# Kernel tuning notes

Hardware: AMD Instinct MI355X
Metric: run time of the kernel (lower is better)

The kernel has to match this reference:

```python
import jax, jax.numpy as jnp
import numpy as np

N = 80000    # total nodes
E = 640000   # total edges
B = 800      # graphs in batch
NPG = 100    # nodes per graph
HID = 128
NC = 10
IND = 20     # one-hot degree feature size (torch.eye(20))
EPS = 1e-5


def _gconv(x, src, dst, inv_out, inv_in, W, b):
    # DGL GraphConv, norm='both': D_out^{-1/2} scaling at src, sum-aggregate, D_in^{-1/2} at dst
    m = (x * inv_out[:, None])[src]                      # [E, F]
    agg = jax.ops.segment_sum(m, dst, num_segments=x.shape[0])
    return (agg * inv_in[:, None]) @ W + b


def _bn(x, gamma, beta):
    # BatchNorm1d, training-mode (batch statistics, biased variance)
    mu = x.mean(0)
    var = x.var(0)
    return (x - mu) / jnp.sqrt(var + EPS) * gamma + beta


def setup_inputs():
    key = jax.random.key(0)
    ks = jax.random.split(key, 10)
    # edges constrained within each graph (batched disjoint graphs, as in dgl.batch)
    eg = jax.random.randint(ks[0], (E,), 0, B)
    src = (eg * NPG + jax.random.randint(ks[1], (E,), 0, NPG)).astype(jnp.int32)
    dst = (eg * NPG + jax.random.randint(ks[2], (E,), 0, NPG)).astype(jnp.int32)
    graph_id = (jnp.arange(N) // NPG).astype(jnp.int32)

    def p(k, shape, fan):
        return (jax.random.normal(k, shape, jnp.float32) / np.sqrt(fan)).astype(jnp.float32)

    z = lambda s: jnp.zeros(s, jnp.float32)
    o = lambda s: jnp.ones(s, jnp.float32)
    return dict(
        src=src, dst=dst, graph_id=graph_id,
        W1=p(ks[3], (IND, HID), IND), b1=z((HID,)), g1=o((HID,)), be1=z((HID,)),
        W2=p(ks[4], (HID, HID), HID), b2=z((HID,)), g2=o((HID,)), be2=z((HID,)),
        Wv=p(ks[5], (HID, 1), HID), bv=z((1,)),
        Wd=p(ks[6], (1, HID), 1), bd=z((HID,)),
        Wg=p(ks[7], (HID, HID), HID), bg=z((HID,)), g3=o((HID,)), be3=z((HID,)),
        Wc=p(ks[8], (HID, NC), HID), bc=z((NC,)),
    )


def reference(src, dst, graph_id, W1, b1, g1, be1, W2, b2, g2, be2,
              Wv, bv, Wd, bd, Wg, bg, g3, be3, Wc, bc):
    n = graph_id.shape[0]
    ones_e = jnp.ones(src.shape[0], jnp.float32)
    in_deg = jax.ops.segment_sum(ones_e, dst, num_segments=n)
    out_deg = jax.ops.segment_sum(ones_e, src, num_segments=n)
    inv_in = jax.lax.rsqrt(jnp.maximum(in_deg, 1.0))   # DGL clamps deg min 1
    inv_out = jax.lax.rsqrt(jnp.maximum(out_deg, 1.0))

    # node features: one-hot of in-degree (eye(20)[in_degrees]); clip to valid range
    h = jax.nn.one_hot(jnp.clip(in_deg.astype(jnp.int32), 0, IND - 1), IND, dtype=jnp.float32)
    h = jax.nn.elu(_bn(_gconv(h, src, dst, inv_out, inv_in, W1, b1), g1, be1))  # [N,HID]
    h = jax.nn.elu(_bn(_gconv(h, src, dst, inv_out, inv_in, W2, b2), g2, be2))  # [N,HID]

    v = _gconv(h, src, dst, inv_out, inv_in, Wv, bv)   # [N,1], node weights d
    d = v[:, 0]

    # per-graph ragged matmul: vec_i = d_i^T @ h_i, done as one segment-sum
    vec = jax.ops.segment_sum(d[:, None] * h, graph_id, num_segments=B).reshape(-1)  # [B*HID]
    mean = vec.mean()
    vec = jax.nn.relu(vec - mean) - jax.nn.relu(-vec - mean)   # soft shrink by global mean

    hg = jnp.tanh(vec.reshape(B, HID))
    hg = jnp.tanh(_bn(hg @ Wg + bg, g3, be3))
    return jnp.tanh(hg @ Wc + bc)   # [B, NC] (eval-mode output)
```

## Files before the change

### kernel.cpp

```cpp
#include <hip/hip_runtime.h>
#include <hip/hip_bf16.h>
#include <math.h>

#define N_NODES 80000
#define N_EDGES 640000
#define B_GR 800
#define NPG 100
#define HID 128
#define NC 10
#define IND 20
#define BN_EPS 1e-5f

__global__ void k_A(const int* __restrict__ src, const int* __restrict__ dst,
                    unsigned int* A) {
    int e = blockIdx.x * blockDim.x + threadIdx.x;
    if (e < N_EDGES) {
        int s = src[e], d = dst[e];
        int g = d / NPG;
        int bidx = g * (NPG * NPG) + (d - g * NPG) * NPG + (s - g * NPG);
        atomicAdd(&A[bidx >> 2], 1u << ((bidx & 3) * 8));
    }
}

__global__ __launch_bounds__(128) void k_prep(const unsigned int* __restrict__ A,
                                              float* __restrict__ inv_in,
                                              float* __restrict__ inv_out,
                                              float* __restrict__ agg20) {
    __shared__ unsigned int s_A[NPG * 25];
    __shared__ float s_io[NPG];
    __shared__ int   s_ix[NPG];
    __shared__ float s_agg[NPG][IND + 1];
    int g = blockIdx.x, gbase = g * NPG, t = threadIdx.x;
    const unsigned int* Ag = A + g * 2500;
    for (int i = t; i < NPG * 25; i += 128) s_A[i] = Ag[i];
    __syncthreads();

    if (t < NPG) {
        int rsum = 0;
        const unsigned int* row = &s_A[t * 25];
#pragma unroll
        for (int q = 0; q < 25; ++q) {
            unsigned int c4 = row[q];
            rsum += (int)((c4 & 255u) + ((c4 >> 8) & 255u) + ((c4 >> 16) & 255u) + (c4 >> 24));
        }
        int csum = 0;
        int wq = t >> 2, sh = (t & 3) * 8;
#pragma unroll 4
        for (int r = 0; r < NPG; ++r)
            csum += (int)((s_A[r * 25 + wq] >> sh) & 255u);

        float io = rsqrtf(fmaxf((float)csum, 1.f));
        inv_in[gbase + t]  = rsqrtf(fmaxf((float)rsum, 1.f));
        inv_out[gbase + t] = io;
        s_io[t] = io;
        s_ix[t] = rsum > IND - 1 ? IND - 1 : rsum;
    }
    __syncthreads();

    if (t < NPG) {
#pragma unroll
        for (int k = 0; k < IND; ++k) s_agg[t][k] = 0.f;
        const unsigned int* row = &s_A[t * 25];
#pragma unroll
        for (int q = 0; q < 25; ++q) {
            unsigned int c4 = row[q];
            if (c4 == 0) continue;
#pragma unroll
            for (int b = 0; b < 4; ++b) {
                unsigned int cnt = (c4 >> (8 * b)) & 255u;
                if (cnt) {
                    int s = q * 4 + b;
                    s_agg[t][s_ix[s]] += (float)cnt * s_io[s];
                }
            }
        }
        float* outp = agg20 + (size_t)(gbase + t) * IND;
#pragma unroll
        for (int k = 0; k < IND; ++k) outp[k] = s_agg[t][k];
    }
}

#define MOM_CHUNK 64
__global__ __launch_bounds__(256) void k_mom(const float* __restrict__ agg20,
                                             const float* __restrict__ inv_in,
                                             float* s20, float* Mbuf) {
    __shared__ float rows[MOM_CHUNK * IND];
    __shared__ float w1s[MOM_CHUNK], w2s[MOM_CHUNK];
    int t = threadIdx.x;
    int k = 0, l = 0;
    bool isM = (t < 210), isS = (t >= 210 && t < 230);
    if (isM) {
        int idx = t, kk = 0;
        while (idx >= IND - kk) { idx -= IND - kk; ++kk; }
        k = kk; l = kk + idx;
    } else if (isS) {
        k = t - 210;
    }
    float acc = 0.f;
    for (int c = blockIdx.x; c < N_NODES / MOM_CHUNK; c += gridDim.x) {
        __syncthreads();
        for (int i = t * 4; i < MOM_CHUNK * IND; i += 1024)
            *(float4*)&rows[i] = *(const float4*)&agg20[(size_t)c * MOM_CHUNK * IND + i];
        if (t < MOM_CHUNK) {
            float v = inv_in[c * MOM_CHUNK + t];
            w1s[t] = v; w2s[t] = v * v;
        }
        __syncthreads();
        if (isM) {
            for (int i = 0; i < MOM_CHUNK; ++i)
                acc += w2s[i] * rows[i * IND + k] * rows[i * IND + l];
        } else if (isS) {
            for (int i = 0; i < MOM_CHUNK; ++i)
                acc += w1s[i] * rows[i * IND + k];
        }
    }
    if (isM) atomicAdd(&Mbuf[t], acc);
    else if (isS) atomicAdd(&s20[t - 210], acc);
}

__global__ void k_bn1fin(const float* __restrict__ s20, const float* __restrict__ Mbuf,
                         const float* __restrict__ W1, const float* __restrict__ b1,
                         const float* __restrict__ g1, const float* __restrict__ be1,
                         float* a1, float* c1) {
    __shared__ float sM[210], ss[IND];
    int j = threadIdx.x;
    if (j < 210) sM[j] = Mbuf[j];
    if (j + 128 < 210) sM[j + 128] = Mbuf[j + 128];
    if (j < IND) ss[j] = s20[j];
    __syncthreads();
    float w[IND];
#pragma unroll
    for (int k = 0; k < IND; ++k) w[k] = W1[k * HID + j];
    float tj = 0.f;
#pragma unroll
    for (int k = 0; k < IND; ++k) tj += ss[k] * w[k];
    float q = 0.f;
    int idx = 0;
#pragma unroll
    for (int k = 0; k < IND; ++k) {
        q += sM[idx] * w[k] * w[k]; ++idx;
#pragma unroll
        for (int l = k + 1; l < IND; ++l) { q += 2.f * sM[idx] * w[k] * w[l]; ++idx; }
    }
    float bj = b1[j];
    const float Nf = (float)N_NODES;
    float mean = (tj + Nf * bj) / Nf;
    float ey2  = (q + 2.f * bj * tj + Nf * bj * bj) / Nf;
    float var  = ey2 - mean * mean;
    float aj = g1[j] / sqrtf(var + BN_EPS);
    a1[j] = aj;
    c1[j] = be1[j] - mean * aj;
}

__global__ __launch_bounds__(256) void k_l1f(const float* __restrict__ agg20,
                                             const float* __restrict__ inv_in,
                                             const float* __restrict__ inv_out,
                                             const float* __restrict__ W1,
                                             const float* __restrict__ b1,
                                             const float* __restrict__ a1,
                                             const float* __restrict__ c1,
                                             float* __restrict__ h1s) {
    __shared__ float ws[IND * HID];
    int t = threadIdx.x;
    for (int i = t * 4; i < IND * HID; i += 1024)
        *(float4*)&ws[i] = *(const float4*)&W1[i];
    __syncthreads();
    int tx = t & 15, ty = t >> 4;
    int c0 = tx * 8;
    float4 ba = *(const float4*)(b1 + c0);
    float4 bb = *(const float4*)(b1 + c0 + 4);
    float4 aa = *(const float4*)(a1 + c0);
    float4 ab = *(const float4*)(a1 + c0 + 4);
    float4 ca = *(const float4*)(c1 + c0);
    float4 cb = *(const float4*)(c1 + c0 + 4);

    int row0 = blockIdx.x * 64 + ty * 4;
    const float* xr0 = agg20 + (size_t)row0 * IND;
    const float* xr1 = xr0 + IND;
    const float* xr2 = xr1 + IND;
    const float* xr3 = xr2 + IND;
    float acc[4][8];
#pragma unroll
    for (int r = 0; r < 4; ++r)
#pragma unroll
        for (int c = 0; c < 8; ++c) acc[r][c] = 0.f;

#pragma unroll
    for (int k = 0; k < IND; k += 4) {
        float4 x0 = *(const float4*)(xr0 + k);
        float4 x1 = *(const float4*)(xr1 + k);
        float4 x2 = *(const float4*)(xr2 + k);
        float4 x3 = *(const float4*)(xr3 + k);
#pragma unroll
        for (int kk = 0; kk < 4; ++kk) {
            float4 wa = *(const float4*)&ws[(k + kk) * HID + c0];
            float4 wb = *(const float4*)&ws[(k + kk) * HID + c0 + 4];
            float xk0 = (kk == 0) ? x0.x : (kk == 1) ? x0.y : (kk == 2) ? x0.z : x0.w;
            float xk1 = (kk == 0) ? x1.x : (kk == 1) ? x1.y : (kk == 2) ? x1.z : x1.w;
            float xk2 = (kk == 0) ? x2.x : (kk == 1) ? x2.y : (kk == 2) ? x2.z : x2.w;
            float xk3 = (kk == 0) ? x3.x : (kk == 1) ? x3.y : (kk == 2) ? x3.z : x3.w;
            acc[0][0] += xk0 * wa.x; acc[0][1] += xk0 * wa.y;
            acc[0][2] += xk0 * wa.z; acc[0][3] += xk0 * wa.w;
            acc[0][4] += xk0 * wb.x; acc[0][5] += xk0 * wb.y;
            acc[0][6] += xk0 * wb.z; acc[0][7] += xk0 * wb.w;
            acc[1][0] += xk1 * wa.x; acc[1][1] += xk1 * wa.y;
            acc[1][2] += xk1 * wa.z; acc[1][3] += xk1 * wa.w;
            acc[1][4] += xk1 * wb.x; acc[1][5] += xk1 * wb.y;
            acc[1][6] += xk1 * wb.z; acc[1][7] += xk1 * wb.w;
            acc[2][0] += xk2 * wa.x; acc[2][1] += xk2 * wa.y;
            acc[2][2] += xk2 * wa.z; acc[2][3] += xk2 * wa.w;
            acc[2][4] += xk2 * wb.x; acc[2][5] += xk2 * wb.y;
            acc[2][6] += xk2 * wb.z; acc[2][7] += xk2 * wb.w;
            acc[3][0] += xk3 * wa.x; acc[3][1] += xk3 * wa.y;
            acc[3][2] += xk3 * wa.z; acc[3][3] += xk3 * wa.w;
            acc[3][4] += xk3 * wb.x; acc[3][5] += xk3 * wb.y;
            acc[3][6] += xk3 * wb.z; acc[3][7] += xk3 * wb.w;
        }
    }
    float4 iv = *(const float4*)(inv_in + row0);
    float4 ov = *(const float4*)(inv_out + row0);
#pragma unroll
    for (int r = 0; r < 4; ++r) {
        float ivr = (r == 0) ? iv.x : (r == 1) ? iv.y : (r == 2) ? iv.z : iv.w;
        float ovr = (r == 0) ? ov.x : (r == 1) ? ov.y : (r == 2) ? ov.z : ov.w;
        float y[8];
        y[0] = acc[r][0] * ivr + ba.x; y[1] = acc[r][1] * ivr + ba.y;
        y[2] = acc[r][2] * ivr + ba.z; y[3] = acc[r][3] * ivr + ba.w;
        y[4] = acc[r][4] * ivr + bb.x; y[5] = acc[r][5] * ivr + bb.y;
        y[6] = acc[r][6] * ivr + bb.z; y[7] = acc[r][7] * ivr + bb.w;
        float z[8];
        z[0] = y[0] * aa.x + ca.x; z[1] = y[1] * aa.y + ca.y;
        z[2] = y[2] * aa.z + ca.z; z[3] = y[3] * aa.w + ca.w;
        z[4] = y[4] * ab.x + cb.x; z[5] = y[5] * ab.y + cb.y;
        z[6] = y[6] * ab.z + cb.z; z[7] = y[7] * ab.w + cb.w;
#pragma unroll
        for (int c = 0; c < 8; ++c) {
            float h = z[c] > 0.f ? z[c] : expm1f(z[c]);
            z[c] = h * ovr;
        }
        float* yr = h1s + (size_t)(row0 + r) * HID + c0;
        *(float4*)yr = make_float4(z[0], z[1], z[2], z[3]);
        *(float4*)(yr + 4) = make_float4(z[4], z[5], z[6], z[7]);
    }
}

__global__ __launch_bounds__(512) void k_agg2v5(const unsigned int* __restrict__ A,
                                                const float* __restrict__ h1s,
                                                float* __restrict__ agg2) {
    __shared__ float sh[NPG * HID];
    int t = threadIdx.x;
    int g = blockIdx.x;
    int gbase = g * NPG;

    const float4* srcp = (const float4*)(h1s + (size_t)gbase * HID);
    float4* shp = (float4*)sh;
    for (int i = t; i < (NPG * HID) / 4; i += 512)
        shp[i] = srcp[i];
    __syncthreads();

    int wv = t >> 6, lane = t & 63;
    const unsigned int* Ag = A + g * 2500;
    for (int r = wv; r < NPG; r += 8) {
        const unsigned int* row = Ag + r * 25;
        unsigned int cq[25];
#pragma unroll
        for (int q = 0; q < 25; ++q) cq[q] = row[q];
        float ax = 0.f, ay = 0.f;
#pragma unroll
        for (int q = 0; q < 25; ++q) {
            unsigned int c4 = cq[q];
            if (c4 == 0) continue;
            int sbase = q * 4;
#pragma unroll
            for (int b = 0; b < 4; ++b) {
                unsigned int cnt = (c4 >> (8 * b)) & 255u;
                if (cnt) {
                    float f = (float)cnt;
                    float2 v = *(const float2*)&sh[(sbase + b) * HID + lane * 2];
                    ax += f * v.x; ay += f * v.y;
                }
            }
        }
        *(float2*)(agg2 + (size_t)(gbase + r) * HID + lane * 2) = make_float2(ax, ay);
    }
}

__global__ void k_bnfin(const float* sums, const float* sqs,
                        const float* gamma, const float* beta,
                        float cnt, float* a, float* c) {
    int j = threadIdx.x;
    float mu  = sums[j] / cnt;
    float var = sqs[j] / cnt - mu * mu;
    float aj  = gamma[j] / sqrtf(var + BN_EPS);
    a[j] = aj;
    c[j] = beta[j] - mu * aj;
}

__global__ __launch_bounds__(512) void k_l2v5(const float* __restrict__ xin,
                                              const float* __restrict__ inv_in,
                                              const float* __restrict__ W,
                                              const float* __restrict__ bvec,
                                              float* __restrict__ yout,
                                              float* sums, float* sqs) {
    __shared__ float ws[HID * 64];
    int t = threadIdx.x;
    int tile = blockIdx.x >> 1;
    int half = blockIdx.x & 1;
    int cbase = half * 64;
    for (int i = t; i < HID * 16; i += 512) {
        int k = i >> 4;
        int c4 = (i & 15) << 2;
        *(float4*)&ws[k * 64 + c4] = *(const float4*)&W[k * HID + cbase + c4];
    }
    __syncthreads();

    int tx = t & 15;
    int ty = t >> 4;
    int c0 = tx * 4;
    float4 ba = *(const float4*)(bvec + cbase + c0);
    float csum[4], csq[4];
#pragma unroll
    for (int c = 0; c < 4; ++c) { csum[c] = 0.f; csq[c] = 0.f; }

    int row0 = tile * 128 + ty * 4;
    const float* xr0 = xin + (size_t)row0 * HID;
    const float* xr1 = xr0 + HID;
    const float* xr2 = xr1 + HID;
    const float* xr3 = xr2 + HID;
    float acc[4][4];
#pragma unroll
    for (int r = 0; r < 4; ++r)
#pragma unroll
        for (int c = 0; c < 4; ++c) acc[r][c] = 0.f;

#pragma unroll 4
    for (int k = 0; k < HID; k += 4) {
        float4 x0 = *(const float4*)(xr0 + k);
        float4 x1 = *(const float4*)(xr1 + k);
        float4 x2 = *(const float4*)(xr2 + k);
        float4 x3 = *(const float4*)(xr3 + k);
#pragma unroll
        for (int kk = 0; kk < 4; ++kk) {
            float4 wa = *(const float4*)&ws[(k + kk) * 64 + c0];
            float xk0 = (kk == 0) ? x0.x : (kk == 1) ? x0.y : (kk == 2) ? x0.z : x0.w;
            float xk1 = (kk == 0) ? x1.x : (kk == 1) ? x1.y : (kk == 2) ? x1.z : x1.w;
            float xk2 = (kk == 0) ? x2.x : (kk == 1) ? x2.y : (kk == 2) ? x2.z : x2.w;
            float xk3 = (kk == 0) ? x3.x : (kk == 1) ? x3.y : (kk == 2) ? x3.z : x3.w;
            acc[0][0] += xk0 * wa.x; acc[0][1] += xk0 * wa.y;
            acc[0][2] += xk0 * wa.z; acc[0][3] += xk0 * wa.w;
            acc[1][0] += xk1 * wa.x; acc[1][1] += xk1 * wa.y;
            acc[1][2] += xk1 * wa.z; acc[1][3] += xk1 * wa.w;
            acc[2][0] += xk2 * wa.x; acc[2][1] += xk2 * wa.y;
            acc[2][2] += xk2 * wa.z; acc[2][3] += xk2 * wa.w;
            acc[3][0] += xk3 * wa.x; acc[3][1] += xk3 * wa.y;
            acc[3][2] += xk3 * wa.z; acc[3][3] += xk3 * wa.w;
        }
    }
    float4 iv = *(const float4*)(inv_in + row0);
#pragma unroll
    for (int r = 0; r < 4; ++r) {
        float ivr = (r == 0) ? iv.x : (r == 1) ? iv.y : (r == 2) ? iv.z : iv.w;
        float y0 = acc[r][0] * ivr + ba.x;
        float y1 = acc[r][1] * ivr + ba.y;
        float y2 = acc[r][2] * ivr + ba.z;
        float y3 = acc[r][3] * ivr + ba.w;
        csum[0] += y0; csq[0] += y0 * y0;
        csum[1] += y1; csq[1] += y1 * y1;
        csum[2] += y2; csq[2] += y2 * y2;
        csum[3] += y3; csq[3] += y3 * y3;
        *(float4*)(yout + (size_t)(row0 + r) * HID + cbase + c0) = make_float4(y0, y1, y2, y3);
    }

    __syncthreads();
#pragma unroll
    for (int c = 0; c < 4; ++c) {
        ws[ty * 64 + c0 + c] = csum[c];
        ws[2048 + ty * 64 + c0 + c] = csq[c];
    }
    __syncthreads();
    if (t < 64) {
        float s1 = 0.f, s2 = 0.f;
#pragma unroll
        for (int r = 0; r < 32; ++r) {
            s1 += ws[r * 64 + t];
            s2 += ws[2048 + r * 64 + t];
        }
        atomicAdd(&sums[cbase + t], s1);
        atomicAdd(&sqs[cbase + t], s2);
    }
}

__global__ __launch_bounds__(512) void k_post(const unsigned int* __restrict__ A,
                                              const float* __restrict__ y2,
                                              const float* __restrict__ a2,
                                              const float* __restrict__ c2,
                                              const float* __restrict__ inv_in,
                                              const float* __restrict__ inv_out,
                                              const float* __restrict__ Wv,
                                              const float* __restrict__ bv,
                                              float* __restrict__ vec,
                                              float* meansum) {
    __shared__ float sh[NPG * HID];
    __shared__ float s_p[NPG];
    __shared__ float s_d[NPG];
    __shared__ float s_red[512];
    int t = threadIdx.x;
    int g = blockIdx.x, gbase = g * NPG;

    const float4* srcp = (const float4*)(y2 + (size_t)gbase * HID);
    for (int i = t; i < (NPG * HID) / 4; i += 512) {
        int col = (i * 4) & (HID - 1);
        float4 v = srcp[i];
        float4 av = *(const float4*)(a2 + col);
        float4 cv = *(const float4*)(c2 + col);
        float z0 = v.x * av.x + cv.x; z0 = z0 > 0.f ? z0 : expm1f(z0);
        float z1 = v.y * av.y + cv.y; z1 = z1 > 0.f ? z1 : expm1f(z1);
        float z2 = v.z * av.z + cv.z; z2 = z2 > 0.f ? z2 : expm1f(z2);
        float z3 = v.w * av.w + cv.w; z3 = z3 > 0.f ? z3 : expm1f(z3);
        *(float4*)&sh[i * 4] = make_float4(z0, z1, z2, z3);
    }
    __syncthreads();

    int wv = t >> 6, lane = t & 63;
    float2 wvv = *(const float2*)(Wv + lane * 2);
    for (int r = wv; r < NPG; r += 8) {
        float2 h = *(const float2*)&sh[r * HID + lane * 2];
        float d = h.x * wvv.x + h.y * wvv.y;
        for (int off = 32; off; off >>= 1) d += __shfl_down(d, off);
        if (lane == 0) s_p[r] = d * inv_out[gbase + r];
    }
    __syncthreads();

    if (t < NPG) {
        const unsigned int* row = A + g * 2500 + t * 25;
        unsigned int cq[25];
#pragma unroll
        for (int q = 0; q < 25; ++q) cq[q] = row[q];
        float acc = 0.f;
#pragma unroll
        for (int q = 0; q < 25; ++q) {
            unsigned int c4 = cq[q];
            if (c4 == 0) continue;
#pragma unroll
            for (int b = 0; b < 4; ++b) {
                unsigned int cnt = (c4 >> (8 * b)) & 255u;
                if (cnt) acc += (float)cnt * s_p[q * 4 + b];
            }
        }
        s_d[t] = acc * inv_in[gbase + t] + bv[0];
    }
    __syncthreads();

    int col = t & (HID - 1);
    int qr = t >> 7;
    float part = 0.f;
    for (int r = qr * 25; r < qr * 25 + 25; ++r)
        part += s_d[r] * sh[r * HID + col];
    s_red[qr * HID + col] = part;
    __syncthreads();
    if (t < HID) {
        float v = s_red[t] + s_red[HID + t] + s_red[2 * HID + t] + s_red[3 * HID + t];
        vec[g * HID + t] = v;
        for (int off = 32; off; off >>= 1) v += __shfl_down(v, off);
        if ((t & 63) == 0) atomicAdd(meansum, v);
    }
}

__global__ __launch_bounds__(128) void k_g1(const float* __restrict__ vec,
                                            const float* __restrict__ meansum,
                                            const float* __restrict__ Wg,
                                            const float* __restrict__ bg,
                                            float* y3, float* sums, float* sqs) {
    __shared__ float ws[HID * HID];
    __shared__ float rows[HID];
    int g = blockIdx.x, j = threadIdx.x;
    for (int k = 0; k < HID; ++k) ws[k * HID + j] = Wg[k * HID + j];
    float mean = meansum[0] * (1.f / (B_GR * HID));
    float v = vec[g * HID + j];
    float sh = fmaxf(v - mean, 0.f) - fmaxf(-v - mean, 0.f);
    rows[j] = tanhf(sh);
    __syncthreads();
    float acc = 0.f;
#pragma unroll 8
    for (int k = 0; k < HID; ++k) acc += rows[k] * ws[k * HID + j];
    float y = acc + bg[j];
    y3[g * HID + j] = y;
    atomicAdd(&sums[j], y);
    atomicAdd(&sqs[j], y * y);
}

__global__ __launch_bounds__(128) void k_out(const float* __restrict__ y3,
                                             const float* __restrict__ a,
                                             const float* __restrict__ c,
                                             const float* __restrict__ Wc,
                                             const float* __restrict__ bc,
                                             float* out) {
    __shared__ float hg[HID];
    int g = blockIdx.x, j = threadIdx.x;
    hg[j] = tanhf(y3[g * HID + j] * a[j] + c[j]);
    __syncthreads();
    if (j < NC) {
        float acc = 0.f;
        for (int k = 0; k < HID; ++k) acc += hg[k] * Wc[k * NC + j];
        out[g * NC + j] = tanhf(acc + bc[j]);
    }
}

extern "C" void kernel_launch(void* const* d_in, const int* in_sizes, int n_in,
                              void* d_out, int out_size, void* d_ws, size_t ws_size,
                              hipStream_t stream) {
    const int*   src = (const int*)d_in[0];
    const int*   dst = (const int*)d_in[1];
    const float* W1  = (const float*)d_in[3];
    const float* b1  = (const float*)d_in[4];
    const float* g1  = (const float*)d_in[5];
    const float* be1 = (const float*)d_in[6];
    const float* W2  = (const float*)d_in[7];
    const float* b2  = (const float*)d_in[8];
    const float* g2  = (const float*)d_in[9];
    const float* be2 = (const float*)d_in[10];
    const float* Wv  = (const float*)d_in[11];
    const float* bv  = (const float*)d_in[12];
    const float* Wg  = (const float*)d_in[15];
    const float* bg  = (const float*)d_in[16];
    const float* g3  = (const float*)d_in[17];
    const float* be3 = (const float*)d_in[18];
    const float* Wc  = (const float*)d_in[19];
    const float* bc  = (const float*)d_in[20];
    float* out = (float*)d_out;

    char* ws = (char*)d_ws;
    size_t off = 0;
    auto carve = [&](size_t bytes) -> char* {
        char* pp = ws + off;
        off = (off + bytes + 255) & ~(size_t)255;
        return pp;
    };
    unsigned int* A = (unsigned int*)carve((size_t)B_GR * NPG * NPG);
    float* stats   = (float*)carve(2048 * 4);
    size_t zbytes = off;
    float* inv_in  = (float*)carve(N_NODES * 4);
    float* inv_out = (float*)carve(N_NODES * 4);
    float* vec     = (float*)carve((size_t)B_GR * HID * 4);
    float* y3      = (float*)carve((size_t)B_GR * HID * 4);
    float* agg20   = (float*)carve((size_t)N_NODES * IND * 4);
    float* bufA    = (float*)carve((size_t)N_NODES * HID * 4);
    float* bufB    = (float*)carve((size_t)N_NODES * HID * 4);

    float* sums2 = stats + 0;    float* sq2 = stats + 128;
    float* a2    = stats + 256;  float* c2  = stats + 384;
    float* sums3 = stats + 512;  float* sq3 = stats + 640;
    float* a3    = stats + 768;  float* c3  = stats + 896;
    float* meansum = stats + 1024;
    float* s20   = stats + 1056;
    float* Mbuf  = stats + 1088;
    float* a1    = stats + 1312;
    float* c1    = stats + 1440;

    hipMemsetAsync(d_ws, 0, zbytes, stream);

    k_A<<<(N_EDGES + 255) / 256, 256, 0, stream>>>(src, dst, A);
    k_prep<<<B_GR, 128, 0, stream>>>(A, inv_in, inv_out, agg20);
    k_mom<<<320, 256, 0, stream>>>(agg20, inv_in, s20, Mbuf);
    k_bn1fin<<<1, 128, 0, stream>>>(s20, Mbuf, W1, b1, g1, be1, a1, c1);
    k_l1f<<<N_NODES / 64, 256, 0, stream>>>(agg20, inv_in, inv_out, W1, b1, a1, c1, bufA);
    k_agg2v5<<<B_GR, 512, 0, stream>>>(A, bufA, bufB);
    k_l2v5<<<(N_NODES / 128) * 2, 512, 0, stream>>>(bufB, inv_in, W2, b2, bufA, sums2, sq2);
    k_bnfin<<<1, 128, 0, stream>>>(sums2, sq2, g2, be2, (float)N_NODES, a2, c2);
    k_post<<<B_GR, 512, 0, stream>>>(A, bufA, a2, c2, inv_in, inv_out, Wv, bv, vec, meansum);
    k_g1<<<B_GR, 128, 0, stream>>>(vec, meansum, Wg, bg, y3, sums3, sq3);
    k_bnfin<<<1, 128, 0, stream>>>(sums3, sq3, g3, be3, (float)B_GR, a3, c3);
    k_out<<<B_GR, 128, 0, stream>>>(y3, a3, c3, Wc, bc, out);
}
```

Before: 284.6 us.

## Run layer-2 GEMM on MFMA with split-bf16 (hi/lo) three-pass emulation

Replaces the FP32 SIMT 128x128 layer-2 matmul with an MFMA bf16 kernel. The aggregation kernel now writes its output as hi and lo bf16 halves, and W2 is pre-packed the same way into the MFMA operand layout. Three MFMAs (hi*hi, hi*lo, lo*hi) approximate FP32 accuracy. The aim is to cut the FP32 ALU cost of the GEMM while keeping memory traffic the same. The cost is an extra packing kernel, slightly lower precision, and per-element shared-memory atomics in the BN statistics reduction.

```diff
diff --git a/kernel.cpp b/kernel.cpp
--- a/kernel.cpp
+++ b/kernel.cpp
@@ -10,6 +10,18 @@
 #define NC 10
 #define IND 20
 #define BN_EPS 1e-5f
+
+typedef __attribute__((ext_vector_type(8))) short bf16x8;
+typedef __attribute__((ext_vector_type(4))) float f32x4;
+
+__device__ __forceinline__ unsigned short f2bf(float f) {
+    unsigned int u = __float_as_uint(f);
+    u = (u + 0x7fffu + ((u >> 16) & 1u)) >> 16;
+    return (unsigned short)u;
+}
+__device__ __forceinline__ float bf2f(unsigned short h) {
+    return __uint_as_float((unsigned int)h << 16);
+}
 
 __global__ void k_A(const int* __restrict__ src, const int* __restrict__ dst,
                     unsigned int* A) {
@@ -246,7 +258,8 @@
 
 __global__ __launch_bounds__(512) void k_agg2v5(const unsigned int* __restrict__ A,
                                                 const float* __restrict__ h1s,
-                                                float* __restrict__ agg2) {
+                                                unsigned short* __restrict__ agg2hi,
+                                                unsigned short* __restrict__ agg2lo) {
     __shared__ float sh[NPG * HID];
     int t = threadIdx.x;
     int g = blockIdx.x;
@@ -281,7 +294,102 @@
                 }
             }
         }
-        *(float2*)(agg2 + (size_t)(gbase + r) * HID + lane * 2) = make_float2(ax, ay);
+        unsigned short hx = f2bf(ax), hy = f2bf(ay);
+        unsigned short lx = f2bf(ax - bf2f(hx)), ly = f2bf(ay - bf2f(hy));
+        size_t o = (size_t)(gbase + r) * HID + lane * 2;
+        *(unsigned int*)(agg2hi + o) = (unsigned int)hx | ((unsigned int)hy << 16);
+        *(unsigned int*)(agg2lo + o) = (unsigned int)lx | ((unsigned int)ly << 16);
+    }
+}
+
+__global__ void k_wpack(const float* __restrict__ W2, unsigned short* __restrict__ Wpack) {
+    int i = blockIdx.x * 256 + threadIdx.x;
+    if (i < 16384) {
+        int j = i & 7, l = (i >> 3) & 63, kc = (i >> 9) & 3, nc = i >> 11;
+        int k = kc * 32 + 8 * (l >> 4) + j;
+        int n = nc * 16 + (l & 15);
+        float w = W2[k * HID + n];
+        unsigned short h = f2bf(w);
+        Wpack[i] = h;
+        Wpack[16384 + i] = f2bf(w - bf2f(h));
+    }
+}
+
+__global__ __launch_bounds__(512) void k_l2mf(const unsigned short* __restrict__ agg2hi,
+                                              const unsigned short* __restrict__ agg2lo,
+                                              const float* __restrict__ inv_in,
+                                              const unsigned short* __restrict__ Wpack,
+                                              const float* __restrict__ b2,
+                                              float* __restrict__ y2,
+                                              float* sums, float* sqs) {
+    __shared__ unsigned short wp[32768];
+    int t = threadIdx.x;
+    for (int i = t; i < 4096; i += 512)
+        ((bf16x8*)wp)[i] = ((const bf16x8*)Wpack)[i];
+    __syncthreads();
+
+    int w = t >> 6, l = t & 63;
+    int lg = l >> 4, lr = l & 15;
+    int row0 = blockIdx.x * 128 + w * 16;
+
+    bf16x8 ah[4], al[4];
+    const unsigned short* ahb = agg2hi + (size_t)(row0 + lr) * HID;
+    const unsigned short* alb = agg2lo + (size_t)(row0 + lr) * HID;
+#pragma unroll
+    for (int kc = 0; kc < 4; ++kc) {
+        ah[kc] = *(const bf16x8*)(ahb + kc * 32 + 8 * lg);
+        al[kc] = *(const bf16x8*)(alb + kc * 32 + 8 * lg);
+    }
+
+    f32x4 acc[8];
+#pragma unroll
+    for (int nc = 0; nc < 8; ++nc) acc[nc] = (f32x4)(0.f);
+#pragma unroll
+    for (int nc = 0; nc < 8; ++nc) {
+#pragma unroll
+        for (int kc = 0; kc < 4; ++kc) {
+            const unsigned short* bp = wp + ((nc * 4 + kc) * 64 + l) * 8;
+            bf16x8 bh = *(const bf16x8*)bp;
+            bf16x8 bl = *(const bf16x8*)(bp + 16384);
+            acc[nc] = __builtin_amdgcn_mfma_f32_16x16x32_bf16(ah[kc], bh, acc[nc], 0, 0, 0);
+            acc[nc] = __builtin_amdgcn_mfma_f32_16x16x32_bf16(ah[kc], bl, acc[nc], 0, 0, 0);
+            acc[nc] = __builtin_amdgcn_mfma_f32_16x16x32_bf16(al[kc], bh, acc[nc], 0, 0, 0);
+        }
+    }
+
+    float iv[4];
+#pragma unroll
+    for (int r = 0; r < 4; ++r) iv[r] = inv_in[row0 + 4 * lg + r];
+    float ys[8][4];
+#pragma unroll
+    for (int nc = 0; nc < 8; ++nc) {
+        int col = nc * 16 + lr;
+        float bj = b2[col];
+#pragma unroll
+        for (int r = 0; r < 4; ++r) {
+            float y = acc[nc][r] * iv[r] + bj;
+            ys[nc][r] = y;
+            y2[(size_t)(row0 + 4 * lg + r) * HID + col] = y;
+        }
+    }
+
+    __syncthreads();
+    float* red = (float*)wp;
+    if (t < 256) red[t] = 0.f;
+    __syncthreads();
+#pragma unroll
+    for (int nc = 0; nc < 8; ++nc) {
+        int col = nc * 16 + lr;
+        float cs = ys[nc][0] + ys[nc][1] + ys[nc][2] + ys[nc][3];
+        float cq = ys[nc][0] * ys[nc][0] + ys[nc][1] * ys[nc][1]
+                 + ys[nc][2] * ys[nc][2] + ys[nc][3] * ys[nc][3];
+        atomicAdd(&red[col], cs);
+        atomicAdd(&red[128 + col], cq);
+    }
+    __syncthreads();
+    if (t < HID) {
+        atomicAdd(&sums[t], red[t]);
+        atomicAdd(&sqs[t], red[128 + t]);
     }
 }
 
@@ -294,100 +402,6 @@
     float aj  = gamma[j] / sqrtf(var + BN_EPS);
     a[j] = aj;
     c[j] = beta[j] - mu * aj;
-}
-
-__global__ __launch_bounds__(512) void k_l2v5(const float* __restrict__ xin,
-                                              const float* __restrict__ inv_in,
-                                              const float* __restrict__ W,
-                                              const float* __restrict__ bvec,
-                                              float* __restrict__ yout,
-                                              float* sums, float* sqs) {
-    __shared__ float ws[HID * 64];
-    int t = threadIdx.x;
-    int tile = blockIdx.x >> 1;
-    int half = blockIdx.x & 1;
-    int cbase = half * 64;
-    for (int i = t; i < HID * 16; i += 512) {
-        int k = i >> 4;
-        int c4 = (i & 15) << 2;
-        *(float4*)&ws[k * 64 + c4] = *(const float4*)&W[k * HID + cbase + c4];
-    }
-    __syncthreads();
-
-    int tx = t & 15;
-    int ty = t >> 4;
-    int c0 = tx * 4;
-    float4 ba = *(const float4*)(bvec + cbase + c0);
-    float csum[4], csq[4];
-#pragma unroll
-    for (int c = 0; c < 4; ++c) { csum[c] = 0.f; csq[c] = 0.f; }
-
-    int row0 = tile * 128 + ty * 4;
-    const float* xr0 = xin + (size_t)row0 * HID;
-    const float* xr1 = xr0 + HID;
-    const float* xr2 = xr1 + HID;
-    const float* xr3 = xr2 + HID;
-    float acc[4][4];
-#pragma unroll
-    for (int r = 0; r < 4; ++r)
-#pragma unroll
-        for (int c = 0; c < 4; ++c) acc[r][c] = 0.f;
-
-#pragma unroll 4
-    for (int k = 0; k < HID; k += 4) {
-        float4 x0 = *(const float4*)(xr0 + k);
-        float4 x1 = *(const float4*)(xr1 + k);
-        float4 x2 = *(const float4*)(xr2 + k);
-        float4 x3 = *(const float4*)(xr3 + k);
-#pragma unroll
-        for (int kk = 0; kk < 4; ++kk) {
-            float4 wa = *(const float4*)&ws[(k + kk) * 64 + c0];
-            float xk0 = (kk == 0) ? x0.x : (kk == 1) ? x0.y : (kk == 2) ? x0.z : x0.w;
-            float xk1 = (kk == 0) ? x1.x : (kk == 1) ? x1.y : (kk == 2) ? x1.z : x1.w;
-            float xk2 = (kk == 0) ? x2.x : (kk == 1) ? x2.y : (kk == 2) ? x2.z : x2.w;
-            float xk3 = (kk == 0) ? x3.x : (kk == 1) ? x3.y : (kk == 2) ? x3.z : x3.w;
-            acc[0][0] += xk0 * wa.x; acc[0][1] += xk0 * wa.y;
-            acc[0][2] += xk0 * wa.z; acc[0][3] += xk0 * wa.w;
-            acc[1][0] += xk1 * wa.x; acc[1][1] += xk1 * wa.y;
-            acc[1][2] += xk1 * wa.z; acc[1][3] += xk1 * wa.w;
-            acc[2][0] += xk2 * wa.x; acc[2][1] += xk2 * wa.y;
-            acc[2][2] += xk2 * wa.z; acc[2][3] += xk2 * wa.w;
-            acc[3][0] += xk3 * wa.x; acc[3][1] += xk3 * wa.y;
-            acc[3][2] += xk3 * wa.z; acc[3][3] += xk3 * wa.w;
-        }
-    }
-    float4 iv = *(const float4*)(inv_in + row0);
-#pragma unroll
-    for (int r = 0; r < 4; ++r) {
-        float ivr = (r == 0) ? iv.x : (r == 1) ? iv.y : (r == 2) ? iv.z : iv.w;
-        float y0 = acc[r][0] * ivr + ba.x;
-        float y1 = acc[r][1] * ivr + ba.y;
-        float y2 = acc[r][2] * ivr + ba.z;
-        float y3 = acc[r][3] * ivr + ba.w;
-        csum[0] += y0; csq[0] += y0 * y0;
-        csum[1] += y1; csq[1] += y1 * y1;
-        csum[2] += y2; csq[2] += y2 * y2;
-        csum[3] += y3; csq[3] += y3 * y3;
-        *(float4*)(yout + (size_t)(row0 + r) * HID + cbase + c0) = make_float4(y0, y1, y2, y3);
-    }
-
-    __syncthreads();
-#pragma unroll
-    for (int c = 0; c < 4; ++c) {
-        ws[ty * 64 + c0 + c] = csum[c];
-        ws[2048 + ty * 64 + c0 + c] = csq[c];
-    }
-    __syncthreads();
-    if (t < 64) {
-        float s1 = 0.f, s2 = 0.f;
-#pragma unroll
-        for (int r = 0; r < 32; ++r) {
-            s1 += ws[r * 64 + t];
-            s2 += ws[2048 + r * 64 + t];
-        }
-        atomicAdd(&sums[cbase + t], s1);
-        atomicAdd(&sqs[cbase + t], s2);
-    }
 }
 
 __global__ __launch_bounds__(512) void k_post(const unsigned int* __restrict__ A,
@@ -545,7 +559,9 @@
     float* y3      = (float*)carve((size_t)B_GR * HID * 4);
     float* agg20   = (float*)carve((size_t)N_NODES * IND * 4);
     float* bufA    = (float*)carve((size_t)N_NODES * HID * 4);
-    float* bufB    = (float*)carve((size_t)N_NODES * HID * 4);
+    unsigned short* agg2hi = (unsigned short*)carve((size_t)N_NODES * HID * 2);
+    unsigned short* agg2lo = (unsigned short*)carve((size_t)N_NODES * HID * 2);
+    unsigned short* Wpack  = (unsigned short*)carve(32768 * 2);
 
     float* sums2 = stats + 0;    float* sq2 = stats + 128;
     float* a2    = stats + 256;  float* c2  = stats + 384;
@@ -560,12 +576,14 @@
     hipMemsetAsync(d_ws, 0, zbytes, stream);
 
     k_A<<<(N_EDGES + 255) / 256, 256, 0, stream>>>(src, dst, A);
+    k_wpack<<<64, 256, 0, stream>>>(W2, Wpack);
     k_prep<<<B_GR, 128, 0, stream>>>(A, inv_in, inv_out, agg20);
     k_mom<<<320, 256, 0, stream>>>(agg20, inv_in, s20, Mbuf);
     k_bn1fin<<<1, 128, 0, stream>>>(s20, Mbuf, W1, b1, g1, be1, a1, c1);
     k_l1f<<<N_NODES / 64, 256, 0, stream>>>(agg20, inv_in, inv_out, W1, b1, a1, c1, bufA);
-    k_agg2v5<<<B_GR, 512, 0, stream>>>(A, bufA, bufB);
-    k_l2v5<<<(N_NODES / 128) * 2, 512, 0, stream>>>(bufB, inv_in, W2, b2, bufA, sums2, sq2);
+    k_agg2v5<<<B_GR, 512, 0, stream>>>(A, bufA, agg2hi, agg2lo);
+    k_l2mf<<<N_NODES / 128, 512, 0, stream>>>(agg2hi, agg2lo, inv_in, Wpack, b2,
+                                              bufA, sums2, sq2);
     k_bnfin<<<1, 128, 0, stream>>>(sums2, sq2, g2, be2, (float)N_NODES, a2, c2);
     k_post<<<B_GR, 512, 0, stream>>>(A, bufA, a2, c2, inv_in, inv_out, Wv, bv, vec, meansum);
     k_g1<<<B_GR, 128, 0, stream>>>(vec, meansum, Wg, bg, y3, sums3, sq3);
```

Result: slower. 292.2 us (+2.6%).

## Build per-graph CSR edge lists in prep and use them in aggregation kernels

Applied to the files above, without the earlier changes.

The prep kernel now prefix-sums per-row nonzero counts and emits a compact per-graph CSR list of (source, count) entries. The layer-2 aggregation and the final post kernel walk these lists instead of scanning the dense byte-packed 100x100 adjacency with branchy unpacking. This cuts wasted loads and divergent branches in the gather loops. In exchange prep gets a block scan and extra global writes, and each graph is capped at 1024 unique edges, which could overflow on denser graphs.

```diff
diff --git a/kernel.cpp b/kernel.cpp
--- a/kernel.cpp
+++ b/kernel.cpp
@@ -10,6 +10,7 @@
 #define NC 10
 #define IND 20
 #define BN_EPS 1e-5f
+#define ENT_CAP 1024
 
 __global__ void k_A(const int* __restrict__ src, const int* __restrict__ dst,
                     unsigned int* A) {
@@ -25,16 +26,20 @@
 __global__ __launch_bounds__(128) void k_prep(const unsigned int* __restrict__ A,
                                               float* __restrict__ inv_in,
                                               float* __restrict__ inv_out,
-                                              float* __restrict__ agg20) {
+                                              float* __restrict__ agg20,
+                                              unsigned int* __restrict__ ent,
+                                              int* __restrict__ goff) {
     __shared__ unsigned int s_A[NPG * 25];
     __shared__ float s_io[NPG];
     __shared__ int   s_ix[NPG];
     __shared__ float s_agg[NPG][IND + 1];
+    __shared__ int s_offs[128];
     int g = blockIdx.x, gbase = g * NPG, t = threadIdx.x;
     const unsigned int* Ag = A + g * 2500;
     for (int i = t; i < NPG * 25; i += 128) s_A[i] = Ag[i];
     __syncthreads();
 
+    int nnz = 0;
     if (t < NPG) {
         int rsum = 0;
         const unsigned int* row = &s_A[t * 25];
@@ -42,6 +47,8 @@
         for (int q = 0; q < 25; ++q) {
             unsigned int c4 = row[q];
             rsum += (int)((c4 & 255u) + ((c4 >> 8) & 255u) + ((c4 >> 16) & 255u) + (c4 >> 24));
+            nnz += (int)((c4 & 255u) != 0) + (int)(((c4 >> 8) & 255u) != 0)
+                 + (int)(((c4 >> 16) & 255u) != 0) + (int)((c4 >> 24) != 0);
         }
         int csum = 0;
         int wq = t >> 2, sh = (t & 3) * 8;
@@ -55,12 +62,26 @@
         s_io[t] = io;
         s_ix[t] = rsum > IND - 1 ? IND - 1 : rsum;
     }
+    int v = nnz;
+    s_offs[t] = v;
+    __syncthreads();
+    for (int d = 1; d < 128; d <<= 1) {
+        int x = (t >= d) ? s_offs[t - d] : 0;
+        __syncthreads();
+        s_offs[t] += x;
+        __syncthreads();
+    }
+    int my_off = s_offs[t] - v;
+    if (t < NPG) goff[g * 104 + t] = my_off;
+    if (t == 0) goff[g * 104 + NPG] = s_offs[127];
     __syncthreads();
 
     if (t < NPG) {
 #pragma unroll
         for (int k = 0; k < IND; ++k) s_agg[t][k] = 0.f;
         const unsigned int* row = &s_A[t * 25];
+        unsigned int* ep = ent + (size_t)g * ENT_CAP + my_off;
+        int w = 0;
 #pragma unroll
         for (int q = 0; q < 25; ++q) {
             unsigned int c4 = row[q];
@@ -71,6 +92,7 @@
                 if (cnt) {
                     int s = q * 4 + b;
                     s_agg[t][s_ix[s]] += (float)cnt * s_io[s];
+                    ep[w++] = ((unsigned int)s << 8) | cnt;
                 }
             }
         }
@@ -244,10 +266,12 @@
     }
 }
 
-__global__ __launch_bounds__(512) void k_agg2v5(const unsigned int* __restrict__ A,
+__global__ __launch_bounds__(512) void k_agg2v6(const unsigned int* __restrict__ ent,
+                                                const int* __restrict__ goff,
                                                 const float* __restrict__ h1s,
                                                 float* __restrict__ agg2) {
     __shared__ float sh[NPG * HID];
+    __shared__ int s_off[NPG + 1];
     int t = threadIdx.x;
     int g = blockIdx.x;
     int gbase = g * NPG;
@@ -256,30 +280,33 @@
     float4* shp = (float4*)sh;
     for (int i = t; i < (NPG * HID) / 4; i += 512)
         shp[i] = srcp[i];
+    if (t <= NPG) s_off[t] = goff[g * 104 + t];
     __syncthreads();
 
     int wv = t >> 6, lane = t & 63;
-    const unsigned int* Ag = A + g * 2500;
+    const unsigned int* ep = ent + (size_t)g * ENT_CAP;
     for (int r = wv; r < NPG; r += 8) {
-        const unsigned int* row = Ag + r * 25;
-        unsigned int cq[25];
-#pragma unroll
-        for (int q = 0; q < 25; ++q) cq[q] = row[q];
+        int e0 = s_off[r], e1 = s_off[r + 1];
         float ax = 0.f, ay = 0.f;
-#pragma unroll
-        for (int q = 0; q < 25; ++q) {
-            unsigned int c4 = cq[q];
-            if (c4 == 0) continue;
-            int sbase = q * 4;
-#pragma unroll
-            for (int b = 0; b < 4; ++b) {
-                unsigned int cnt = (c4 >> (8 * b)) & 255u;
-                if (cnt) {
-                    float f = (float)cnt;
-                    float2 v = *(const float2*)&sh[(sbase + b) * HID + lane * 2];
-                    ax += f * v.x; ay += f * v.y;
-                }
+        int i = e0;
+        for (; i + 8 <= e1; i += 8) {
+            unsigned int ee[8];
+#pragma unroll
+            for (int j = 0; j < 8; ++j) ee[j] = ep[i + j];
+#pragma unroll
+            for (int j = 0; j < 8; ++j) {
+                float f = (float)(ee[j] & 255u);
+                int s = ee[j] >> 8;
+                float2 v = *(const float2*)&sh[s * HID + lane * 2];
+                ax += f * v.x; ay += f * v.y;
             }
+        }
+        for (; i < e1; ++i) {
+            unsigned int e = ep[i];
+            float f = (float)(e & 255u);
+            int s = e >> 8;
+            float2 v = *(const float2*)&sh[s * HID + lane * 2];
+            ax += f * v.x; ay += f * v.y;
         }
         *(float2*)(agg2 + (size_t)(gbase + r) * HID + lane * 2) = make_float2(ax, ay);
     }
@@ -390,7 +417,8 @@
     }
 }
 
-__global__ __launch_bounds__(512) void k_post(const unsigned int* __restrict__ A,
+__global__ __launch_bounds__(512) void k_post(const unsigned int* __restrict__ ent,
+                                              const int* __restrict__ goff,
                                               const float* __restrict__ y2,
                                               const float* __restrict__ a2,
                                               const float* __restrict__ c2,
@@ -404,6 +432,7 @@
     __shared__ float s_p[NPG];
     __shared__ float s_d[NPG];
     __shared__ float s_red[512];
+    __shared__ int s_off[NPG + 1];
     int t = threadIdx.x;
     int g = blockIdx.x, gbase = g * NPG;
 
@@ -419,6 +448,7 @@
         float z3 = v.w * av.w + cv.w; z3 = z3 > 0.f ? z3 : expm1f(z3);
         *(float4*)&sh[i * 4] = make_float4(z0, z1, z2, z3);
     }
+    if (t <= NPG) s_off[t] = goff[g * 104 + t];
     __syncthreads();
 
     int wv = t >> 6, lane = t & 63;
@@ -432,20 +462,12 @@
     __syncthreads();
 
     if (t < NPG) {
-        const unsigned int* row = A + g * 2500 + t * 25;
-        unsigned int cq[25];
-#pragma unroll
-        for (int q = 0; q < 25; ++q) cq[q] = row[q];
+        const unsigned int* ep = ent + (size_t)g * ENT_CAP;
+        int e0 = s_off[t], e1 = s_off[t + 1];
         float acc = 0.f;
-#pragma unroll
-        for (int q = 0; q < 25; ++q) {
-            unsigned int c4 = cq[q];
-            if (c4 == 0) continue;
-#pragma unroll
-            for (int b = 0; b < 4; ++b) {
-                unsigned int cnt = (c4 >> (8 * b)) & 255u;
-                if (cnt) acc += (float)cnt * s_p[q * 4 + b];
-            }
+        for (int i = e0; i < e1; ++i) {
+            unsigned int e = ep[i];
+            acc += (float)(e & 255u) * s_p[e >> 8];
         }
         s_d[t] = acc * inv_in[gbase + t] + bv[0];
     }
@@ -546,6 +568,8 @@
     float* agg20   = (float*)carve((size_t)N_NODES * IND * 4);
     float* bufA    = (float*)carve((size_t)N_NODES * HID * 4);
     float* bufB    = (float*)carve((size_t)N_NODES * HID * 4);
+    unsigned int* ent = (unsigned int*)carve((size_t)B_GR * ENT_CAP * 4);
+    int* goff      = (int*)carve((size_t)B_GR * 104 * 4);
 
     float* sums2 = stats + 0;    float* sq2 = stats + 128;
     float* a2    = stats + 256;  float* c2  = stats + 384;
@@ -560,14 +584,15 @@
     hipMemsetAsync(d_ws, 0, zbytes, stream);
 
     k_A<<<(N_EDGES + 255) / 256, 256, 0, stream>>>(src, dst, A);
-    k_prep<<<B_GR, 128, 0, stream>>>(A, inv_in, inv_out, agg20);
+    k_prep<<<B_GR, 128, 0, stream>>>(A, inv_in, inv_out, agg20, ent, goff);
     k_mom<<<320, 256, 0, stream>>>(agg20, inv_in, s20, Mbuf);
     k_bn1fin<<<1, 128, 0, stream>>>(s20, Mbuf, W1, b1, g1, be1, a1, c1);
     k_l1f<<<N_NODES / 64, 256, 0, stream>>>(agg20, inv_in, inv_out, W1, b1, a1, c1, bufA);
-    k_agg2v5<<<B_GR, 512, 0, stream>>>(A, bufA, bufB);
+    k_agg2v6<<<B_GR, 512, 0, stream>>>(ent, goff, bufA, bufB);
     k_l2v5<<<(N_NODES / 128) * 2, 512, 0, stream>>>(bufB, inv_in, W2, b2, bufA, sums2, sq2);
     k_bnfin<<<1, 128, 0, stream>>>(sums2, sq2, g2, be2, (float)N_NODES, a2, c2);
-    k_post<<<B_GR, 512, 0, stream>>>(A, bufA, a2, c2, inv_in, inv_out, Wv, bv, vec, meansum);
+    k_post<<<B_GR, 512, 0, stream>>>(ent, goff, bufA, a2, c2, inv_in, inv_out, Wv, bv,
+                                     vec, meansum);
     k_g1<<<B_GR, 128, 0, stream>>>(vec, meansum, Wg, bg, y3, sums3, sq3);
     k_bnfin<<<1, 128, 0, stream>>>(sums3, sq3, g3, be3, (float)B_GR, a3, c3);
     k_out<<<B_GR, 128, 0, stream>>>(y3, a3, c3, Wc, bc, out);
```

New measurement: 270.0 us, median of 2. 5.1% less time.
